# Kernel optimization log

Measured on AMD Instinct MI355X. Metric: run time of the kernel, lower is better.

The kernel has to match this reference:

```python
import jax, jax.numpy as jnp
import numpy as np

N_HEAD = 16
N_KV_HEAD = 4
HEAD_DIM = 64  # n_embd // n_head = 1024 // 16
N_EMBD = 1024


def _alibi_bias(T, n_head, head_dim):
    # slopes: start = 2**(-2**(-(log2(H)-3))); slope_i = start**(i+1)
    start = 2.0 ** (-2.0 ** (-(np.log2(n_head) - 3.0)))
    slopes = jnp.asarray(start ** np.arange(1, n_head + 1), dtype=jnp.float32)  # [H]
    rel = (jnp.arange(T, dtype=jnp.float32)[None, :]
           - jnp.arange(T, dtype=jnp.float32)[:, None])  # [T,T], rel[i,j] = j - i
    bias = slopes[:, None, None] * rel[None, :, :]  # [H,T,T]
    # Faithful to the torch module: masked_fill(-inf) is then OVERWRITTEN by
    # torch.tril, which zeroes the upper triangle. Net effect: lower-tri alibi
    # values, 0 above the diagonal (NO causal masking).
    bias = jnp.tril(bias)
    return bias * (head_dim ** -0.5)  # extra scale applied in forward


def setup_inputs() -> dict:
    key = jax.random.key(0)
    ks = jax.random.split(key, 5)
    B, T, C = 4, 2048, N_EMBD
    w_scale = 0.02
    return {
        "x": jax.random.normal(ks[0], (B, T, C), dtype=jnp.float32),
        "Wq": jax.random.normal(ks[1], (C, C), dtype=jnp.float32) * w_scale,
        "Wkv": jax.random.normal(ks[2], (2 * N_KV_HEAD * HEAD_DIM, C), dtype=jnp.float32) * w_scale,
        "Wproj": jax.random.normal(ks[3], (C, C), dtype=jnp.float32) * w_scale,
        "bproj": jnp.zeros((C,), dtype=jnp.float32),
    }


def reference(x, Wq, Wkv, Wproj, bproj):
    B, T, C = x.shape
    H, KVH, D = N_HEAD, N_KV_HEAD, HEAD_DIM
    ratio = H // KVH

    q = jnp.einsum('btc,ec->bte', x, Wq).reshape(B, T, H, D).transpose(0, 2, 1, 3)  # [B,H,T,D]
    kv = jnp.einsum('btc,ec->bte', x, Wkv)  # [B,T,2*KVH*D]
    k, v = jnp.split(kv, 2, axis=-1)
    k = k.reshape(B, T, KVH, D).transpose(0, 2, 1, 3)  # [B,KVH,T,D]
    v = v.reshape(B, T, KVH, D).transpose(0, 2, 1, 3)
    # torch .repeat tiles whole blocks: query head h uses kv head h % KVH
    k = jnp.tile(k, (1, ratio, 1, 1))  # [B,H,T,D]
    v = jnp.tile(v, (1, ratio, 1, 1))

    bias = _alibi_bias(T, H, D)  # [H,T,T], already *= D**-0.5
    scores = jnp.einsum('bhtd,bhsd->bhts', q, k) * (D ** -0.5) + bias[None]
    attn = jax.nn.softmax(scores, axis=-1)
    out = jnp.einsum('bhts,bhsd->bhtd', attn, v)  # [B,H,T,D]
    out = out.transpose(0, 2, 1, 3).reshape(B, T, C)
    return jnp.einsum('btc,ec->bte', out, Wproj) + bproj
```

## Files before the change

### kernel.cpp

```cpp
#include <hip/hip_runtime.h>
#include <hip/hip_bf16.h>
#include <cstdint>

typedef __bf16 bf16;
typedef bf16 bf16x2 __attribute__((ext_vector_type(2)));
typedef bf16 bf16x4 __attribute__((ext_vector_type(4)));
typedef bf16 bf16x8 __attribute__((ext_vector_type(8)));
typedef float f32x4 __attribute__((ext_vector_type(4)));
typedef unsigned int uint32x2_t __attribute__((ext_vector_type(2)));
typedef unsigned int uint32x4_t __attribute__((ext_vector_type(4)));

#define MFMA16(a, b, c) __builtin_amdgcn_mfma_f32_16x16x32_bf16((a), (b), (c), 0, 0, 0)

#define QSCALE 0.18033688011112042f

__device__ inline void async16(const bf16* g, bf16* l) {
  __builtin_amdgcn_global_load_lds(
      (const __attribute__((address_space(1))) void*)g,
      (__attribute__((address_space(3))) void*)l, 16, 0, 0);
}

__global__ void cast_all(const float* __restrict__ x, const float* __restrict__ wq,
                         const float* __restrict__ wkv, const float* __restrict__ wp,
                         bf16* __restrict__ xb, bf16* __restrict__ w1b,
                         bf16* __restrict__ wpb) {
  const int i = blockIdx.x * blockDim.x + threadIdx.x;
  const float4* src;
  bf16x4* dst;
  int idx;
  if (i < 2097152) {
    src = (const float4*)x; dst = (bf16x4*)xb; idx = i;
  } else if (i < 2359296) {
    src = (const float4*)wq; dst = (bf16x4*)w1b; idx = i - 2097152;
  } else if (i < 2490368) {
    src = (const float4*)wkv; dst = (bf16x4*)(w1b + 1048576); idx = i - 2359296;
  } else {
    src = (const float4*)wp; dst = (bf16x4*)wpb; idx = i - 2490368;
  }
  const float4 v = src[idx];
  bf16x4 o;
  o.x = (bf16)v.x; o.y = (bf16)v.y; o.z = (bf16)v.z; o.w = (bf16)v.w;
  dst[idx] = o;
}

__global__ __launch_bounds__(256, 2)
void gemm_qkv(const bf16* __restrict__ A, const bf16* __restrict__ B,
              bf16* __restrict__ qb, bf16* __restrict__ kb, bf16* __restrict__ vb) {
  constexpr int K = 1024;
  __shared__ bf16 sA[128 * 64];
  __shared__ bf16 sB[128 * 64];
  const int tid = threadIdx.x;
  const int lane = tid & 63, wid = tid >> 6;
  const int col = lane & 15, quad = lane >> 4;
  const int wm = wid >> 1, wn = wid & 1;
  const int m0 = blockIdx.y * 128, n0 = blockIdx.x * 128;
  const int c7 = col & 7;

  f32x4 acc[4][4];
  const f32x4 z = {0.f, 0.f, 0.f, 0.f};
#pragma unroll
  for (int mi = 0; mi < 4; mi++)
#pragma unroll
    for (int ni = 0; ni < 4; ni++) acc[mi][ni] = z;

  for (int k0 = 0; k0 < K; k0 += 64) {
    __syncthreads();
#pragma unroll
    for (int c = 0; c < 4; ++c) {
      const int idx = c * 256 + tid;
      const int row = idx >> 3, kc = idx & 7;
      const int gkc = kc ^ (row & 7);
      async16(&A[(size_t)(m0 + row) * K + k0 + gkc * 8], &sA[idx * 8]);
      async16(&B[(size_t)(n0 + row) * K + k0 + gkc * 8], &sB[idx * 8]);
    }
    __syncthreads();
#pragma unroll
    for (int ks = 0; ks < 2; ++ks) {
      bf16x8 af[4], bfr[4];
#pragma unroll
      for (int i = 0; i < 4; i++)
        af[i] = *(const bf16x8*)&sA[(wm * 64 + i * 16 + col) * 64 +
                                    (((ks * 4 + quad) ^ c7) << 3)];
#pragma unroll
      for (int i = 0; i < 4; i++)
        bfr[i] = *(const bf16x8*)&sB[(wn * 64 + i * 16 + col) * 64 +
                                     (((ks * 4 + quad) ^ c7) << 3)];
#pragma unroll
      for (int mi = 0; mi < 4; mi++)
#pragma unroll
        for (int ni = 0; ni < 4; ni++)
          acc[mi][ni] = MFMA16(af[mi], bfr[ni], acc[mi][ni]);
    }
  }
#pragma unroll
  for (int mi = 0; mi < 4; mi++) {
#pragma unroll
    for (int ni = 0; ni < 4; ni++) {
      const int e = n0 + wn * 64 + ni * 16 + col;
#pragma unroll
      for (int r = 0; r < 4; r++) {
        const int m = m0 + wm * 64 + mi * 16 + quad * 4 + r;
        const int bb = m >> 11, t = m & 2047;
        if (e < 1024) {
          qb[(((size_t)bb * 16 + (e >> 6)) * 2048 + t) * 64 + (e & 63)] =
              (bf16)(acc[mi][ni][r] * QSCALE);
        } else if (e < 1280) {
          const int f = e - 1024;
          kb[(((size_t)bb * 4 + (f >> 6)) * 2048 + t) * 64 + (f & 63)] =
              (bf16)acc[mi][ni][r];
        } else {
          const int f = e - 1280;
          vb[(((size_t)bb * 4 + (f >> 6)) * 2048 + t) * 64 + (f & 63)] =
              (bf16)acc[mi][ni][r];
        }
      }
    }
  }
}

__global__ __launch_bounds__(256, 2)
void gemm_proj(const bf16* __restrict__ A, const bf16* __restrict__ B,
               const float* __restrict__ bias, float* __restrict__ out) {
  constexpr int K = 1024;
  __shared__ bf16 sA[128 * 64];
  __shared__ bf16 sB[128 * 64];
  const int tid = threadIdx.x;
  const int lane = tid & 63, wid = tid >> 6;
  const int col = lane & 15, quad = lane >> 4;
  const int wm = wid >> 1, wn = wid & 1;
  const int m0 = blockIdx.y * 128, n0 = blockIdx.x * 128;
  const int c7 = col & 7;

  f32x4 acc[4][4];
  const f32x4 z = {0.f, 0.f, 0.f, 0.f};
#pragma unroll
  for (int mi = 0; mi < 4; mi++)
#pragma unroll
    for (int ni = 0; ni < 4; ni++) acc[mi][ni] = z;

  for (int k0 = 0; k0 < K; k0 += 64) {
    __syncthreads();
#pragma unroll
    for (int c = 0; c < 4; ++c) {
      const int idx = c * 256 + tid;
      const int row = idx >> 3, kc = idx & 7;
      const int gkc = kc ^ (row & 7);
      async16(&A[(size_t)(m0 + row) * K + k0 + gkc * 8], &sA[idx * 8]);
      async16(&B[(size_t)(n0 + row) * K + k0 + gkc * 8], &sB[idx * 8]);
    }
    __syncthreads();
#pragma unroll
    for (int ks = 0; ks < 2; ++ks) {
      bf16x8 af[4], bfr[4];
#pragma unroll
      for (int i = 0; i < 4; i++)
        af[i] = *(const bf16x8*)&sA[(wm * 64 + i * 16 + col) * 64 +
                                    (((ks * 4 + quad) ^ c7) << 3)];
#pragma unroll
      for (int i = 0; i < 4; i++)
        bfr[i] = *(const bf16x8*)&sB[(wn * 64 + i * 16 + col) * 64 +
                                     (((ks * 4 + quad) ^ c7) << 3)];
#pragma unroll
      for (int mi = 0; mi < 4; mi++)
#pragma unroll
        for (int ni = 0; ni < 4; ni++)
          acc[mi][ni] = MFMA16(af[mi], bfr[ni], acc[mi][ni]);
    }
  }
#pragma unroll
  for (int mi = 0; mi < 4; mi++) {
#pragma unroll
    for (int ni = 0; ni < 4; ni++) {
      const int e = n0 + wn * 64 + ni * 16 + col;
      const float be = bias[e];
#pragma unroll
      for (int r = 0; r < 4; r++) {
        const int m = m0 + wm * 64 + mi * 16 + quad * 4 + r;
        out[(size_t)m * 1024 + e] = acc[mi][ni][r] + be;
      }
    }
  }
}

__global__ __launch_bounds__(256, 2)
void attn_alibi(const bf16* __restrict__ qb, const bf16* __restrict__ kb,
                const bf16* __restrict__ vb, bf16* __restrict__ ob) {
  __shared__ bf16 sK[2][64 * 64];
  __shared__ bf16 sVt[2][64 * 72];
  const int tid = threadIdx.x;
  const int lane = tid & 63, wid = tid >> 6;
  const int col = lane & 15, quad = lane >> 4;
  const int c7 = col & 7;
  const int bh = blockIdx.y;
  const int b = bh >> 4, h = bh & 15, kvh = h & 3;
  const int qbase = __builtin_amdgcn_readfirstlane(blockIdx.x * 256 + wid * 64);

  const bf16* qptr = qb + ((size_t)(b * 16 + h) * 2048 + qbase) * 64;
  const bf16* kptr = kb + ((size_t)(b * 4 + kvh) * 2048) * 64;
  const bf16* vptr = vb + ((size_t)(b * 4 + kvh) * 2048) * 64;

  bf16x8 bq[4][2];
#pragma unroll
  for (int ni = 0; ni < 4; ni++)
#pragma unroll
    for (int ks = 0; ks < 2; ks++)
      bq[ni][ks] = *(const bf16x8*)&qptr[(ni * 16 + col) * 64 + ks * 32 + quad * 8];

  bf16x8 bones;
#pragma unroll
  for (int j = 0; j < 8; j++) bones[j] = (bf16)1.0f;

  f32x4 O[4][4];
  f32x4 Osum[4];
  const f32x4 z = {0.f, 0.f, 0.f, 0.f};
#pragma unroll
  for (int mi = 0; mi < 4; mi++) {
    Osum[mi] = z;
#pragma unroll
    for (int nd = 0; nd < 4; nd++) O[mi][nd] = z;
  }

  const float cb = exp2f(-0.5f * (float)(h + 1)) * QSCALE;
  const int qoff = quad * 4 - col;

  const int rowA = tid >> 3, kc = tid & 7;
  const int kxA = (kc ^ (rowA & 7)) << 3;
  const int rv = rowA * 2;
  const int blkv = rv >> 3, rlv = rv & 7;

  async16(&kptr[(size_t)rowA * 64 + kxA], &sK[0][tid * 8]);
  async16(&kptr[(size_t)(rowA + 32) * 64 + kxA], &sK[0][(256 + tid) * 8]);
  bf16x8 vr0 = *(const bf16x8*)&vptr[(size_t)rv * 64 + kc * 8];
  bf16x8 vr1 = *(const bf16x8*)&vptr[(size_t)(rv + 1) * 64 + kc * 8];

  int bufi = 0;
  for (int c0 = 0; c0 < 2048; c0 += 64, bufi ^= 1) {
    bf16* skw = sK[bufi];
    bf16* svw = sVt[bufi];
#pragma unroll
    for (int j = 0; j < 8; j++) {
      bf16x2 pr;
      pr.x = vr0[j];
      pr.y = vr1[j];
      *(bf16x2*)&svw[(kc * 8 + j) * 72 + ((blkv ^ kc) << 3) + rlv] = pr;
    }
    __syncthreads();

    {
      const int cn = (c0 + 64 < 2048) ? c0 + 64 : 0;
      bf16* skn = sK[bufi ^ 1];
      async16(&kptr[(size_t)(cn + rowA) * 64 + kxA], &skn[tid * 8]);
      async16(&kptr[(size_t)(cn + rowA + 32) * 64 + kxA], &skn[(256 + tid) * 8]);
      vr0 = *(const bf16x8*)&vptr[(size_t)(cn + rv) * 64 + kc * 8];
      vr1 = *(const bf16x8*)&vptr[(size_t)(cn + rv + 1) * 64 + kc * 8];
    }

    f32x4 S[4][4];
#pragma unroll
    for (int mi = 0; mi < 4; mi++)
#pragma unroll
      for (int ni = 0; ni < 4; ni++) S[mi][ni] = z;
#pragma unroll
    for (int ks = 0; ks < 2; ks++) {
      bf16x8 ak[4];
#pragma unroll
      for (int mi = 0; mi < 4; mi++)
        ak[mi] = *(const bf16x8*)&skw[(mi * 16 + col) * 64 +
                                      (((ks * 4 + quad) ^ c7) << 3)];
#pragma unroll
      for (int mi = 0; mi < 4; mi++)
#pragma unroll
        for (int ni = 0; ni < 4; ni++)
          S[mi][ni] = MFMA16(ak[mi], bq[ni][ks], S[mi][ni]);
    }

    bf16x8 ap[4][2];
#pragma unroll
    for (int ni = 0; ni < 4; ni++) {
#pragma unroll
      for (int ks = 0; ks < 2; ks++) {
        unsigned plo[2], phi[2];
#pragma unroll
        for (int t = 0; t < 2; t++) {
          const int mi = ks * 2 + t;
          const int U = c0 + mi * 16 - qbase - ni * 16;
          f32x4 p;
          if (U <= -15) {
            const float bb = cb * (float)(U + qoff);
#pragma unroll
            for (int r = 0; r < 4; r++)
              p[r] = __builtin_amdgcn_exp2f(S[mi][ni][r] + (bb + cb * (float)r));
          } else if (U >= 16) {
#pragma unroll
            for (int r = 0; r < 4; r++)
              p[r] = __builtin_amdgcn_exp2f(S[mi][ni][r]);
          } else {
            const float relf = (float)(U + qoff);
#pragma unroll
            for (int r = 0; r < 4; r++) {
              const float rr = relf + (float)r;
              const float bb = (rr <= 0.f) ? cb * rr : 0.f;
              p[r] = __builtin_amdgcn_exp2f(S[mi][ni][r] + bb);
            }
          }
          bf16x2 lo, hi;
          lo.x = (bf16)p[0]; lo.y = (bf16)p[1];
          hi.x = (bf16)p[2]; hi.y = (bf16)p[3];
          plo[t] = __builtin_bit_cast(unsigned, lo);
          phi[t] = __builtin_bit_cast(unsigned, hi);
        }
        uint32x2_t rl = __builtin_amdgcn_permlane32_swap(plo[0], plo[1], false, false);
        uint32x2_t rh = __builtin_amdgcn_permlane32_swap(phi[0], phi[1], false, false);
        uint32x2_t w02 = __builtin_amdgcn_permlane16_swap(rl.x, rl.y, false, false);
        uint32x2_t w13 = __builtin_amdgcn_permlane16_swap(rh.x, rh.y, false, false);
        uint32x4_t W;
        W.x = w02.x; W.y = w13.x; W.z = w02.y; W.w = w13.y;
        ap[ni][ks] = __builtin_bit_cast(bf16x8, W);
      }
    }

#pragma unroll
    for (int ks = 0; ks < 2; ks++) {
      bf16x8 bv[4];
#pragma unroll
      for (int nd = 0; nd < 4; nd++) {
        const int d = nd * 16 + col;
        bv[nd] = *(const bf16x8*)&svw[d * 72 + (((ks * 4 + quad) ^ (d >> 3)) << 3)];
      }
#pragma unroll
      for (int mi = 0; mi < 4; mi++) {
#pragma unroll
        for (int nd = 0; nd < 4; nd++)
          O[mi][nd] = MFMA16(ap[mi][ks], bv[nd], O[mi][nd]);
        Osum[mi] = MFMA16(ap[mi][ks], bones, Osum[mi]);
      }
    }
  }

#pragma unroll
  for (int mi = 0; mi < 4; mi++) {
#pragma unroll
    for (int r = 0; r < 4; r++) {
      const float inv = 1.0f / Osum[mi][r];
      const int t = qbase + mi * 16 + quad * 4 + r;
#pragma unroll
      for (int nd = 0; nd < 4; nd++) {
        ob[((size_t)b * 2048 + t) * 1024 + h * 64 + nd * 16 + col] =
            (bf16)(O[mi][nd][r] * inv);
      }
    }
  }
}

extern "C" void kernel_launch(void* const* d_in, const int* in_sizes, int n_in,
                              void* d_out, int out_size, void* d_ws, size_t ws_size,
                              hipStream_t stream) {
  const float* x     = (const float*)d_in[0];
  const float* Wq    = (const float*)d_in[1];
  const float* Wkv   = (const float*)d_in[2];
  const float* Wproj = (const float*)d_in[3];
  const float* bproj = (const float*)d_in[4];
  float* out = (float*)d_out;

  bf16* xb  = (bf16*)d_ws;
  bf16* w1b = xb  + 8388608;
  bf16* wpb = w1b + 1572864;
  bf16* qb  = wpb + 1048576;
  bf16* kb  = qb  + 8388608;
  bf16* vb  = kb  + 2097152;
  bf16* aob = vb  + 2097152;

  cast_all<<<10752, 256, 0, stream>>>(x, Wq, Wkv, Wproj, xb, w1b, wpb);
  gemm_qkv<<<dim3(12, 64), 256, 0, stream>>>(xb, w1b, qb, kb, vb);
  attn_alibi<<<dim3(8, 64), 256, 0, stream>>>(qb, kb, vb, aob);
  gemm_proj<<<dim3(8, 64), 256, 0, stream>>>(aob, wpb, bproj, out);
}
```

Measured before the change: 254.5 us.

## Halve per-wave query tile in attention to raise occupancy, add MFMA priority hints

Each wave in the attention kernel now processes 32 queries instead of 64. This halves the O, S and Q register footprint, lets launch bounds target 4 blocks per CU, and doubles the grid to 1024 blocks. The kernel also wraps its MFMA sequences in s_setprio to favour matrix issue. The trade-off is that every K/V tile loaded into LDS is reused by half as many queries, so LDS and global traffic for K/V per unit of work doubles.

```diff
diff --git a/kernel.cpp b/kernel.cpp
--- a/kernel.cpp
+++ b/kernel.cpp
@@ -182,7 +182,7 @@
   }
 }
 
-__global__ __launch_bounds__(256, 2)
+__global__ __launch_bounds__(256, 4)
 void attn_alibi(const bf16* __restrict__ qb, const bf16* __restrict__ kb,
                 const bf16* __restrict__ vb, bf16* __restrict__ ob) {
   __shared__ bf16 sK[2][64 * 64];
@@ -193,15 +193,15 @@
   const int c7 = col & 7;
   const int bh = blockIdx.y;
   const int b = bh >> 4, h = bh & 15, kvh = h & 3;
-  const int qbase = __builtin_amdgcn_readfirstlane(blockIdx.x * 256 + wid * 64);
+  const int qbase = __builtin_amdgcn_readfirstlane(blockIdx.x * 128 + wid * 32);
 
   const bf16* qptr = qb + ((size_t)(b * 16 + h) * 2048 + qbase) * 64;
   const bf16* kptr = kb + ((size_t)(b * 4 + kvh) * 2048) * 64;
   const bf16* vptr = vb + ((size_t)(b * 4 + kvh) * 2048) * 64;
 
-  bf16x8 bq[4][2];
-#pragma unroll
-  for (int ni = 0; ni < 4; ni++)
+  bf16x8 bq[2][2];
+#pragma unroll
+  for (int ni = 0; ni < 2; ni++)
 #pragma unroll
     for (int ks = 0; ks < 2; ks++)
       bq[ni][ks] = *(const bf16x8*)&qptr[(ni * 16 + col) * 64 + ks * 32 + quad * 8];
@@ -210,14 +210,14 @@
 #pragma unroll
   for (int j = 0; j < 8; j++) bones[j] = (bf16)1.0f;
 
-  f32x4 O[4][4];
-  f32x4 Osum[4];
+  f32x4 O[2][4];
+  f32x4 Osum[2];
   const f32x4 z = {0.f, 0.f, 0.f, 0.f};
 #pragma unroll
-  for (int mi = 0; mi < 4; mi++) {
-    Osum[mi] = z;
-#pragma unroll
-    for (int nd = 0; nd < 4; nd++) O[mi][nd] = z;
+  for (int qi = 0; qi < 2; qi++) {
+    Osum[qi] = z;
+#pragma unroll
+    for (int nd = 0; nd < 4; nd++) O[qi][nd] = z;
   }
 
   const float cb = exp2f(-0.5f * (float)(h + 1)) * QSCALE;
@@ -255,28 +255,34 @@
       vr1 = *(const bf16x8*)&vptr[(size_t)(cn + rv + 1) * 64 + kc * 8];
     }
 
-    f32x4 S[4][4];
-#pragma unroll
-    for (int mi = 0; mi < 4; mi++)
-#pragma unroll
-      for (int ni = 0; ni < 4; ni++) S[mi][ni] = z;
-#pragma unroll
-    for (int ks = 0; ks < 2; ks++) {
+    f32x4 S[4][2];
+    {
       bf16x8 ak[4];
 #pragma unroll
       for (int mi = 0; mi < 4; mi++)
-        ak[mi] = *(const bf16x8*)&skw[(mi * 16 + col) * 64 +
-                                      (((ks * 4 + quad) ^ c7) << 3)];
-#pragma unroll
-      for (int mi = 0; mi < 4; mi++)
-#pragma unroll
-        for (int ni = 0; ni < 4; ni++)
-          S[mi][ni] = MFMA16(ak[mi], bq[ni][ks], S[mi][ni]);
-    }
-
-    bf16x8 ap[4][2];
-#pragma unroll
-    for (int ni = 0; ni < 4; ni++) {
+        ak[mi] = *(const bf16x8*)&skw[(mi * 16 + col) * 64 + ((quad ^ c7) << 3)];
+      __builtin_amdgcn_s_setprio(1);
+#pragma unroll
+      for (int mi = 0; mi < 4; mi++)
+#pragma unroll
+        for (int ni = 0; ni < 2; ni++)
+          S[mi][ni] = MFMA16(ak[mi], bq[ni][0], z);
+      __builtin_amdgcn_s_setprio(0);
+#pragma unroll
+      for (int mi = 0; mi < 4; mi++)
+        ak[mi] = *(const bf16x8*)&skw[(mi * 16 + col) * 64 + (((4 + quad) ^ c7) << 3)];
+      __builtin_amdgcn_s_setprio(1);
+#pragma unroll
+      for (int mi = 0; mi < 4; mi++)
+#pragma unroll
+        for (int ni = 0; ni < 2; ni++)
+          S[mi][ni] = MFMA16(ak[mi], bq[ni][1], S[mi][ni]);
+      __builtin_amdgcn_s_setprio(0);
+    }
+
+    bf16x8 ap[2][2];
+#pragma unroll
+    for (int ni = 0; ni < 2; ni++) {
 #pragma unroll
       for (int ks = 0; ks < 2; ks++) {
         unsigned plo[2], phi[2];
@@ -327,26 +333,28 @@
         const int d = nd * 16 + col;
         bv[nd] = *(const bf16x8*)&svw[d * 72 + (((ks * 4 + quad) ^ (d >> 3)) << 3)];
       }
-#pragma unroll
-      for (int mi = 0; mi < 4; mi++) {
+      __builtin_amdgcn_s_setprio(1);
+#pragma unroll
+      for (int qi = 0; qi < 2; qi++) {
 #pragma unroll
         for (int nd = 0; nd < 4; nd++)
-          O[mi][nd] = MFMA16(ap[mi][ks], bv[nd], O[mi][nd]);
-        Osum[mi] = MFMA16(ap[mi][ks], bones, Osum[mi]);
-      }
-    }
-  }
-
-#pragma unroll
-  for (int mi = 0; mi < 4; mi++) {
+          O[qi][nd] = MFMA16(ap[qi][ks], bv[nd], O[qi][nd]);
+        Osum[qi] = MFMA16(ap[qi][ks], bones, Osum[qi]);
+      }
+      __builtin_amdgcn_s_setprio(0);
+    }
+  }
+
+#pragma unroll
+  for (int qi = 0; qi < 2; qi++) {
 #pragma unroll
     for (int r = 0; r < 4; r++) {
-      const float inv = 1.0f / Osum[mi][r];
-      const int t = qbase + mi * 16 + quad * 4 + r;
+      const float inv = 1.0f / Osum[qi][r];
+      const int t = qbase + qi * 16 + quad * 4 + r;
 #pragma unroll
       for (int nd = 0; nd < 4; nd++) {
         ob[((size_t)b * 2048 + t) * 1024 + h * 64 + nd * 16 + col] =
-            (bf16)(O[mi][nd][r] * inv);
+            (bf16)(O[qi][nd][r] * inv);
       }
     }
   }
@@ -372,6 +380,6 @@
 
   cast_all<<<10752, 256, 0, stream>>>(x, Wq, Wkv, Wproj, xb, w1b, wpb);
   gemm_qkv<<<dim3(12, 64), 256, 0, stream>>>(xb, w1b, qb, kb, vb);
-  attn_alibi<<<dim3(8, 64), 256, 0, stream>>>(qb, kb, vb, aob);
+  attn_alibi<<<dim3(16, 64), 256, 0, stream>>>(qb, kb, vb, aob);
   gemm_proj<<<dim3(8, 64), 256, 0, stream>>>(aob, wpb, bproj, out);
 }
```

Measured after the change: 252.3 us. No clear change (-0.8%).

## Split attention over two KV halves and combine partials in a separate kernel

Applied to the files above, without the earlier changes.

Attention now runs over two halves of the key/value sequence in separate blocks (grid z=2). Each block writes unnormalized fp32 partial outputs and row sums, and a new combine kernel adds the two halves, normalizes, and writes bf16. This is meant to double the block count for better CU occupancy, and launch bounds are raised to 4 blocks per SM. The diff also adds s_setprio around the MFMA bursts and drops the S zero-init by passing zero as the accumulator. The cost is extra fp32 global traffic of about 64MB written and then read, plus one more launch; softmax needs no max-rescaling because no running max is kept.

```diff
diff --git a/kernel.cpp b/kernel.cpp
--- a/kernel.cpp
+++ b/kernel.cpp
@@ -182,9 +182,10 @@
   }
 }
 
-__global__ __launch_bounds__(256, 2)
+__global__ __launch_bounds__(256, 4)
 void attn_alibi(const bf16* __restrict__ qb, const bf16* __restrict__ kb,
-                const bf16* __restrict__ vb, bf16* __restrict__ ob) {
+                const bf16* __restrict__ vb, float* __restrict__ po,
+                float* __restrict__ ps) {
   __shared__ bf16 sK[2][64 * 64];
   __shared__ bf16 sVt[2][64 * 72];
   const int tid = threadIdx.x;
@@ -193,6 +194,8 @@
   const int c7 = col & 7;
   const int bh = blockIdx.y;
   const int b = bh >> 4, h = bh & 15, kvh = h & 3;
+  const int kvsplit = blockIdx.z;
+  const int kbeg = kvsplit << 10, kend = kbeg + 1024;
   const int qbase = __builtin_amdgcn_readfirstlane(blockIdx.x * 256 + wid * 64);
 
   const bf16* qptr = qb + ((size_t)(b * 16 + h) * 2048 + qbase) * 64;
@@ -228,13 +231,13 @@
   const int rv = rowA * 2;
   const int blkv = rv >> 3, rlv = rv & 7;
 
-  async16(&kptr[(size_t)rowA * 64 + kxA], &sK[0][tid * 8]);
-  async16(&kptr[(size_t)(rowA + 32) * 64 + kxA], &sK[0][(256 + tid) * 8]);
-  bf16x8 vr0 = *(const bf16x8*)&vptr[(size_t)rv * 64 + kc * 8];
-  bf16x8 vr1 = *(const bf16x8*)&vptr[(size_t)(rv + 1) * 64 + kc * 8];
+  async16(&kptr[(size_t)(kbeg + rowA) * 64 + kxA], &sK[0][tid * 8]);
+  async16(&kptr[(size_t)(kbeg + rowA + 32) * 64 + kxA], &sK[0][(256 + tid) * 8]);
+  bf16x8 vr0 = *(const bf16x8*)&vptr[(size_t)(kbeg + rv) * 64 + kc * 8];
+  bf16x8 vr1 = *(const bf16x8*)&vptr[(size_t)(kbeg + rv + 1) * 64 + kc * 8];
 
   int bufi = 0;
-  for (int c0 = 0; c0 < 2048; c0 += 64, bufi ^= 1) {
+  for (int c0 = kbeg; c0 < kend; c0 += 64, bufi ^= 1) {
     bf16* skw = sK[bufi];
     bf16* svw = sVt[bufi];
 #pragma unroll
@@ -247,7 +250,7 @@
     __syncthreads();
 
     {
-      const int cn = (c0 + 64 < 2048) ? c0 + 64 : 0;
+      const int cn = (c0 + 64 < kend) ? c0 + 64 : kbeg;
       bf16* skn = sK[bufi ^ 1];
       async16(&kptr[(size_t)(cn + rowA) * 64 + kxA], &skn[tid * 8]);
       async16(&kptr[(size_t)(cn + rowA + 32) * 64 + kxA], &skn[(256 + tid) * 8]);
@@ -256,22 +259,28 @@
     }
 
     f32x4 S[4][4];
-#pragma unroll
-    for (int mi = 0; mi < 4; mi++)
-#pragma unroll
-      for (int ni = 0; ni < 4; ni++) S[mi][ni] = z;
-#pragma unroll
-    for (int ks = 0; ks < 2; ks++) {
+    {
       bf16x8 ak[4];
 #pragma unroll
       for (int mi = 0; mi < 4; mi++)
-        ak[mi] = *(const bf16x8*)&skw[(mi * 16 + col) * 64 +
-                                      (((ks * 4 + quad) ^ c7) << 3)];
+        ak[mi] = *(const bf16x8*)&skw[(mi * 16 + col) * 64 + ((quad ^ c7) << 3)];
+      __builtin_amdgcn_s_setprio(1);
 #pragma unroll
       for (int mi = 0; mi < 4; mi++)
 #pragma unroll
         for (int ni = 0; ni < 4; ni++)
-          S[mi][ni] = MFMA16(ak[mi], bq[ni][ks], S[mi][ni]);
+          S[mi][ni] = MFMA16(ak[mi], bq[ni][0], z);
+      __builtin_amdgcn_s_setprio(0);
+#pragma unroll
+      for (int mi = 0; mi < 4; mi++)
+        ak[mi] = *(const bf16x8*)&skw[(mi * 16 + col) * 64 + (((4 + quad) ^ c7) << 3)];
+      __builtin_amdgcn_s_setprio(1);
+#pragma unroll
+      for (int mi = 0; mi < 4; mi++)
+#pragma unroll
+        for (int ni = 0; ni < 4; ni++)
+          S[mi][ni] = MFMA16(ak[mi], bq[ni][1], S[mi][ni]);
+      __builtin_amdgcn_s_setprio(0);
     }
 
     bf16x8 ap[4][2];
@@ -327,6 +336,7 @@
         const int d = nd * 16 + col;
         bv[nd] = *(const bf16x8*)&svw[d * 72 + (((ks * 4 + quad) ^ (d >> 3)) << 3)];
       }
+      __builtin_amdgcn_s_setprio(1);
 #pragma unroll
       for (int mi = 0; mi < 4; mi++) {
 #pragma unroll
@@ -334,22 +344,44 @@
           O[mi][nd] = MFMA16(ap[mi][ks], bv[nd], O[mi][nd]);
         Osum[mi] = MFMA16(ap[mi][ks], bones, Osum[mi]);
       }
-    }
-  }
-
+      __builtin_amdgcn_s_setprio(0);
+    }
+  }
+
+  float* pob = po + ((size_t)(kvsplit * 64 + bh) * 2048) * 64;
+  float* psb = ps + (size_t)(kvsplit * 64 + bh) * 2048;
 #pragma unroll
   for (int mi = 0; mi < 4; mi++) {
 #pragma unroll
     for (int r = 0; r < 4; r++) {
-      const float inv = 1.0f / Osum[mi][r];
       const int t = qbase + mi * 16 + quad * 4 + r;
+      if (col == 0) psb[t] = Osum[mi][r];
 #pragma unroll
       for (int nd = 0; nd < 4; nd++) {
-        ob[((size_t)b * 2048 + t) * 1024 + h * 64 + nd * 16 + col] =
-            (bf16)(O[mi][nd][r] * inv);
-      }
-    }
-  }
+        pob[(size_t)t * 64 + nd * 16 + col] = O[mi][nd][r];
+      }
+    }
+  }
+}
+
+__global__ void combine_o(const float* __restrict__ po, const float* __restrict__ ps,
+                          bf16* __restrict__ ob) {
+  const int i = blockIdx.x * 256 + threadIdx.x;
+  const int dq = i & 15;
+  const int t = (i >> 4) & 2047;
+  const int bh = i >> 15;
+  const size_t base0 = ((size_t)bh * 2048 + t) * 64 + dq * 4;
+  const size_t base1 = ((size_t)(64 + bh) * 2048 + t) * 64 + dq * 4;
+  const float4 a = *(const float4*)&po[base0];
+  const float4 c = *(const float4*)&po[base1];
+  const float inv = 1.0f / (ps[bh * 2048 + t] + ps[(64 + bh) * 2048 + t]);
+  bf16x4 o;
+  o.x = (bf16)((a.x + c.x) * inv);
+  o.y = (bf16)((a.y + c.y) * inv);
+  o.z = (bf16)((a.z + c.z) * inv);
+  o.w = (bf16)((a.w + c.w) * inv);
+  const int b = bh >> 4, h = bh & 15;
+  *(bf16x4*)&ob[((size_t)b * 2048 + t) * 1024 + h * 64 + dq * 4] = o;
 }
 
 extern "C" void kernel_launch(void* const* d_in, const int* in_sizes, int n_in,
@@ -369,9 +401,12 @@
   bf16* kb  = qb  + 8388608;
   bf16* vb  = kb  + 2097152;
   bf16* aob = vb  + 2097152;
+  float* po = (float*)(aob + 8388608);
+  float* ps = po + 16777216;
 
   cast_all<<<10752, 256, 0, stream>>>(x, Wq, Wkv, Wproj, xb, w1b, wpb);
   gemm_qkv<<<dim3(12, 64), 256, 0, stream>>>(xb, w1b, qb, kb, vb);
-  attn_alibi<<<dim3(8, 64), 256, 0, stream>>>(qb, kb, vb, aob);
+  attn_alibi<<<dim3(8, 64, 2), 256, 0, stream>>>(qb, kb, vb, po, ps);
+  combine_o<<<8192, 256, 0, stream>>>(po, ps, aob);
   gemm_proj<<<dim3(8, 64), 256, 0, stream>>>(aob, wpb, bproj, out);
 }
```

Result: slower. 759.0 us (+198.3%).

## Software-pipeline attention loop: overlap previous tile's PV with current QK and softmax

Applied to the files above, without the earlier changes.

Restructures the attention main loop so the PV MFMAs for the previous KV tile are interleaved with the QK MFMAs and exp2 softmax of the current tile, split into two half-strips. V tiles move to a triple LDS buffer so the previous tile's V stays valid while the next one is written. A prologue and epilogue handle the first QK/softmax and the last PV, and s_setprio hints raise wave priority around the MFMA bursts. The aim is to hide transcendental and permute latency behind matrix work. In exchange it uses more LDS and keeps more registers live, which may put the two-blocks-per-CU occupancy target at risk.

```diff
diff --git a/kernel.cpp b/kernel.cpp
--- a/kernel.cpp
+++ b/kernel.cpp
@@ -182,11 +182,103 @@
   }
 }
 
+#define COMMIT_V(svc_)                                                      \
+  _Pragma("unroll")                                                         \
+  for (int j = 0; j < 8; j++) {                                             \
+    bf16x2 pr; pr.x = vr0[j]; pr.y = vr1[j];                                \
+    *(bf16x2*)&(svc_)[(kc * 8 + j) * 72 + ((blkv ^ kc) << 3) + rlv] = pr;   \
+  }
+
+#define QK_STRIP(Sx_, mb_)                                                  \
+  {                                                                         \
+    bf16x8 ak0[2], ak1[2];                                                  \
+    _Pragma("unroll")                                                       \
+    for (int t = 0; t < 2; t++) {                                           \
+      ak0[t] = *(const bf16x8*)&skw[(((mb_) + t) * 16 + col) * 64 +         \
+                                    ((quad ^ c7) << 3)];                    \
+      ak1[t] = *(const bf16x8*)&skw[(((mb_) + t) * 16 + col) * 64 +         \
+                                    (((4 + quad) ^ c7) << 3)];              \
+    }                                                                       \
+    __builtin_amdgcn_s_setprio(1);                                          \
+    _Pragma("unroll")                                                       \
+    for (int t = 0; t < 2; t++)                                             \
+      _Pragma("unroll")                                                     \
+      for (int ni = 0; ni < 4; ni++)                                        \
+        Sx_[t][ni] = MFMA16(ak0[t], bq[ni][0], z);                          \
+    _Pragma("unroll")                                                       \
+    for (int t = 0; t < 2; t++)                                             \
+      _Pragma("unroll")                                                     \
+      for (int ni = 0; ni < 4; ni++)                                        \
+        Sx_[t][ni] = MFMA16(ak1[t], bq[ni][1], Sx_[t][ni]);                 \
+    __builtin_amdgcn_s_setprio(0);                                          \
+  }
+
+#define PV_KS(kspv_, svp_)                                                  \
+  {                                                                         \
+    bf16x8 bv[4];                                                           \
+    _Pragma("unroll")                                                       \
+    for (int nd = 0; nd < 4; nd++) {                                        \
+      const int d = nd * 16 + col;                                          \
+      bv[nd] = *(const bf16x8*)&(svp_)[d * 72 +                             \
+                   ((((kspv_) * 4 + quad) ^ (d >> 3)) << 3)];               \
+    }                                                                       \
+    __builtin_amdgcn_s_setprio(1);                                          \
+    _Pragma("unroll")                                                       \
+    for (int mi = 0; mi < 4; mi++) {                                        \
+      _Pragma("unroll")                                                     \
+      for (int nd = 0; nd < 4; nd++)                                        \
+        O[mi][nd] = MFMA16(ap[mi][kspv_], bv[nd], O[mi][nd]);               \
+      Osum[mi] = MFMA16(ap[mi][kspv_], bones, Osum[mi]);                    \
+    }                                                                       \
+    __builtin_amdgcn_s_setprio(0);                                          \
+  }
+
+#define SM_STRIP(Sx_, mb_, kspv_)                                           \
+  _Pragma("unroll")                                                         \
+  for (int ni = 0; ni < 4; ni++) {                                          \
+    unsigned plo[2], phi[2];                                                \
+    _Pragma("unroll")                                                       \
+    for (int t = 0; t < 2; t++) {                                           \
+      const int U = c0 + ((mb_) + t) * 16 - qbase - ni * 16;                \
+      f32x4 p;                                                              \
+      if (U <= -15) {                                                       \
+        const float bb = cb * (float)(U + qoff);                            \
+        _Pragma("unroll")                                                   \
+        for (int r = 0; r < 4; r++)                                         \
+          p[r] = __builtin_amdgcn_exp2f(Sx_[t][ni][r] + (bb + cb * (float)r)); \
+      } else if (U >= 16) {                                                 \
+        _Pragma("unroll")                                                   \
+        for (int r = 0; r < 4; r++)                                         \
+          p[r] = __builtin_amdgcn_exp2f(Sx_[t][ni][r]);                     \
+      } else {                                                              \
+        const float relf = (float)(U + qoff);                               \
+        _Pragma("unroll")                                                   \
+        for (int r = 0; r < 4; r++) {                                       \
+          const float rr = relf + (float)r;                                 \
+          const float bb = (rr <= 0.f) ? cb * rr : 0.f;                     \
+          p[r] = __builtin_amdgcn_exp2f(Sx_[t][ni][r] + bb);                \
+        }                                                                   \
+      }                                                                     \
+      bf16x2 lo, hi;                                                        \
+      lo.x = (bf16)p[0]; lo.y = (bf16)p[1];                                 \
+      hi.x = (bf16)p[2]; hi.y = (bf16)p[3];                                 \
+      plo[t] = __builtin_bit_cast(unsigned, lo);                            \
+      phi[t] = __builtin_bit_cast(unsigned, hi);                            \
+    }                                                                       \
+    uint32x2_t rl = __builtin_amdgcn_permlane32_swap(plo[0], plo[1], false, false); \
+    uint32x2_t rh = __builtin_amdgcn_permlane32_swap(phi[0], phi[1], false, false); \
+    uint32x2_t w02 = __builtin_amdgcn_permlane16_swap(rl.x, rl.y, false, false);    \
+    uint32x2_t w13 = __builtin_amdgcn_permlane16_swap(rh.x, rh.y, false, false);    \
+    uint32x4_t W;                                                           \
+    W.x = w02.x; W.y = w13.x; W.z = w02.y; W.w = w13.y;                     \
+    ap[ni][kspv_] = __builtin_bit_cast(bf16x8, W);                          \
+  }
+
 __global__ __launch_bounds__(256, 2)
 void attn_alibi(const bf16* __restrict__ qb, const bf16* __restrict__ kb,
                 const bf16* __restrict__ vb, bf16* __restrict__ ob) {
   __shared__ bf16 sK[2][64 * 64];
-  __shared__ bf16 sVt[2][64 * 72];
+  __shared__ bf16 sVt[3][64 * 72];
   const int tid = threadIdx.x;
   const int lane = tid & 63, wid = tid >> 6;
   const int col = lane & 15, quad = lane >> 4;
@@ -233,17 +325,30 @@
   bf16x8 vr0 = *(const bf16x8*)&vptr[(size_t)rv * 64 + kc * 8];
   bf16x8 vr1 = *(const bf16x8*)&vptr[(size_t)(rv + 1) * 64 + kc * 8];
 
-  int bufi = 0;
-  for (int c0 = 0; c0 < 2048; c0 += 64, bufi ^= 1) {
-    bf16* skw = sK[bufi];
-    bf16* svw = sVt[bufi];
-#pragma unroll
-    for (int j = 0; j < 8; j++) {
-      bf16x2 pr;
-      pr.x = vr0[j];
-      pr.y = vr1[j];
-      *(bf16x2*)&svw[(kc * 8 + j) * 72 + ((blkv ^ kc) << 3) + rlv] = pr;
-    }
+  bf16x8 ap[4][2];
+
+  {
+    const int c0 = 0;
+    COMMIT_V(sVt[0]);
+    __syncthreads();
+    async16(&kptr[(size_t)(64 + rowA) * 64 + kxA], &sK[1][tid * 8]);
+    async16(&kptr[(size_t)(64 + rowA + 32) * 64 + kxA], &sK[1][(256 + tid) * 8]);
+    vr0 = *(const bf16x8*)&vptr[(size_t)(64 + rv) * 64 + kc * 8];
+    vr1 = *(const bf16x8*)&vptr[(size_t)(64 + rv + 1) * 64 + kc * 8];
+
+    const bf16* skw = sK[0];
+    f32x4 Sa[2][4], Sb[2][4];
+    QK_STRIP(Sa, 0);
+    SM_STRIP(Sa, 0, 0);
+    QK_STRIP(Sb, 2);
+    SM_STRIP(Sb, 2, 1);
+  }
+
+  int bufi = 1, ivc = 1, ivp = 0;
+  for (int c0 = 64; c0 < 2048; c0 += 64) {
+    const bf16* skw = sK[bufi];
+    const bf16* svp = sVt[ivp];
+    COMMIT_V(sVt[ivc]);
     __syncthreads();
 
     {
@@ -255,86 +360,23 @@
       vr1 = *(const bf16x8*)&vptr[(size_t)(cn + rv + 1) * 64 + kc * 8];
     }
 
-    f32x4 S[4][4];
-#pragma unroll
-    for (int mi = 0; mi < 4; mi++)
-#pragma unroll
-      for (int ni = 0; ni < 4; ni++) S[mi][ni] = z;
-#pragma unroll
-    for (int ks = 0; ks < 2; ks++) {
-      bf16x8 ak[4];
-#pragma unroll
-      for (int mi = 0; mi < 4; mi++)
-        ak[mi] = *(const bf16x8*)&skw[(mi * 16 + col) * 64 +
-                                      (((ks * 4 + quad) ^ c7) << 3)];
-#pragma unroll
-      for (int mi = 0; mi < 4; mi++)
-#pragma unroll
-        for (int ni = 0; ni < 4; ni++)
-          S[mi][ni] = MFMA16(ak[mi], bq[ni][ks], S[mi][ni]);
-    }
-
-    bf16x8 ap[4][2];
-#pragma unroll
-    for (int ni = 0; ni < 4; ni++) {
-#pragma unroll
-      for (int ks = 0; ks < 2; ks++) {
-        unsigned plo[2], phi[2];
-#pragma unroll
-        for (int t = 0; t < 2; t++) {
-          const int mi = ks * 2 + t;
-          const int U = c0 + mi * 16 - qbase - ni * 16;
-          f32x4 p;
-          if (U <= -15) {
-            const float bb = cb * (float)(U + qoff);
-#pragma unroll
-            for (int r = 0; r < 4; r++)
-              p[r] = __builtin_amdgcn_exp2f(S[mi][ni][r] + (bb + cb * (float)r));
-          } else if (U >= 16) {
-#pragma unroll
-            for (int r = 0; r < 4; r++)
-              p[r] = __builtin_amdgcn_exp2f(S[mi][ni][r]);
-          } else {
-            const float relf = (float)(U + qoff);
-#pragma unroll
-            for (int r = 0; r < 4; r++) {
-              const float rr = relf + (float)r;
-              const float bb = (rr <= 0.f) ? cb * rr : 0.f;
-              p[r] = __builtin_amdgcn_exp2f(S[mi][ni][r] + bb);
-            }
-          }
-          bf16x2 lo, hi;
-          lo.x = (bf16)p[0]; lo.y = (bf16)p[1];
-          hi.x = (bf16)p[2]; hi.y = (bf16)p[3];
-          plo[t] = __builtin_bit_cast(unsigned, lo);
-          phi[t] = __builtin_bit_cast(unsigned, hi);
-        }
-        uint32x2_t rl = __builtin_amdgcn_permlane32_swap(plo[0], plo[1], false, false);
-        uint32x2_t rh = __builtin_amdgcn_permlane32_swap(phi[0], phi[1], false, false);
-        uint32x2_t w02 = __builtin_amdgcn_permlane16_swap(rl.x, rl.y, false, false);
-        uint32x2_t w13 = __builtin_amdgcn_permlane16_swap(rh.x, rh.y, false, false);
-        uint32x4_t W;
-        W.x = w02.x; W.y = w13.x; W.z = w02.y; W.w = w13.y;
-        ap[ni][ks] = __builtin_bit_cast(bf16x8, W);
-      }
-    }
-
-#pragma unroll
-    for (int ks = 0; ks < 2; ks++) {
-      bf16x8 bv[4];
-#pragma unroll
-      for (int nd = 0; nd < 4; nd++) {
-        const int d = nd * 16 + col;
-        bv[nd] = *(const bf16x8*)&svw[d * 72 + (((ks * 4 + quad) ^ (d >> 3)) << 3)];
-      }
-#pragma unroll
-      for (int mi = 0; mi < 4; mi++) {
-#pragma unroll
-        for (int nd = 0; nd < 4; nd++)
-          O[mi][nd] = MFMA16(ap[mi][ks], bv[nd], O[mi][nd]);
-        Osum[mi] = MFMA16(ap[mi][ks], bones, Osum[mi]);
-      }
-    }
+    f32x4 Sa[2][4], Sb[2][4];
+    QK_STRIP(Sa, 0);
+    PV_KS(0, svp);
+    SM_STRIP(Sa, 0, 0);
+    QK_STRIP(Sb, 2);
+    PV_KS(1, svp);
+    SM_STRIP(Sb, 2, 1);
+
+    bufi ^= 1;
+    ivp = ivc;
+    ivc = (ivc == 2) ? 0 : ivc + 1;
+  }
+
+  {
+    const bf16* svp = sVt[ivp];
+    PV_KS(0, svp);
+    PV_KS(1, svp);
   }
 
 #pragma unroll
```

After: 239.7 us. 1.06x faster.
